# Kernel tuning notes

Measured on AMD Instinct MI355X. Metric: run time of the kernel, lower is better.

The kernel has to match this reference:

```python
import jax, jax.numpy as jnp
import numpy as np

N, D, H, T = 262144, 128, 256, 4  # nodes, embed_dim, hidden_dim, num node types


def setup_inputs() -> dict:
    key = jax.random.key(0)
    ks = jax.random.split(key, 5)
    h = jax.random.normal(ks[0], (N, D), dtype=jnp.float32)
    message = jax.random.normal(ks[1], (N, D), dtype=jnp.float32)
    node_type_ids = jax.random.randint(ks[2], (N,), 0, T, dtype=jnp.int32)
    # Spectrally-normalized linear weights are just fixed matrices at eval time;
    # scale so spectral norm is O(1).
    W1 = jax.random.normal(ks[3], (T, 2 * D, H), dtype=jnp.float32) / np.sqrt(2 * D)
    b1 = jnp.zeros((T, H), dtype=jnp.float32)
    W2 = jax.random.normal(ks[4], (T, H, D), dtype=jnp.float32) / np.sqrt(H)
    b2 = jnp.zeros((T, D), dtype=jnp.float32)
    return {"h": h, "message": message, "node_type_ids": node_type_ids,
            "W1": W1, "b1": b1, "W2": W2, "b2": b2}


def reference(h, message, node_type_ids, W1, b1, W2, b2):
    # x : (N, 2d) concatenated node state and message
    x = jnp.concatenate([h, message], axis=-1)
    dh = jnp.zeros_like(h)
    # Loop over the small fixed set of node types (T=4); each iteration is a
    # dense 2-layer SiLU MLP, results routed back by boolean mask (the torch
    # code's gather -> MLP -> scatter, expressed as compute-all + select).
    for t in range(T):
        y = jax.nn.silu(x @ W1[t] + b1[t]) @ W2[t] + b2[t]  # (N, d)
        mask = (node_type_ids == t)[:, None]
        dh = jnp.where(mask, y, dh)
    return dh
```

## Files before the change

### kernel.cpp

```cpp
#include <hip/hip_runtime.h>
#include <hip/hip_bf16.h>
#include <stdint.h>

#define N_NODES 262144
#define DDIM 128
#define KDIM 256
#define HDIM 256
#define NTYPE 4
#define BM 64
#define NB 1024

typedef float  f32x4  __attribute__((ext_vector_type(4)));
typedef short  bf16x8 __attribute__((ext_vector_type(8)));
typedef unsigned short u16x4 __attribute__((ext_vector_type(4)));


__device__ __forceinline__ unsigned short f2b(float v) {
    unsigned int u = __builtin_bit_cast(unsigned int, v);
    u += 0x7FFFu + ((u >> 16) & 1u);
    return (unsigned short)(u >> 16);
}

__global__ void k_prep_hist(const int* __restrict__ ids,
                            const float* __restrict__ W1, const float* __restrict__ W2,
                            int* __restrict__ bcnt,
                            unsigned short* __restrict__ W1T, unsigned short* __restrict__ W2T) {
    __shared__ int cnt[NTYPE];
    if (blockIdx.x < NB) {
        int tid = threadIdx.x, lane = tid & 63;
        if (tid < NTYPE) cnt[tid] = 0;
        __syncthreads();
        int t = ids[blockIdx.x * 256 + tid];
        #pragma unroll
        for (int tt = 0; tt < NTYPE; ++tt) {
            unsigned long long m = __ballot(t == tt);
            if (lane == 0) atomicAdd(&cnt[tt], (int)__popcll(m));
        }
        __syncthreads();
        if (tid < NTYPE) bcnt[tid * NB + blockIdx.x] = cnt[tid];
    } else {
        int tid = (blockIdx.x - NB) * 256 + threadIdx.x;
        const int stride = 256 * 256;
        const int n1 = NTYPE * HDIM * KDIM;
        for (int i = tid; i < n1; i += stride) {
            int t = i / (HDIM * KDIM);
            int rem = i % (HDIM * KDIM);
            int hh = rem / KDIM;
            int k  = rem % KDIM;
            W1T[i] = f2b(W1[((size_t)t * KDIM + k) * HDIM + hh]);
        }
        const int n2 = NTYPE * DDIM * HDIM;
        for (int i = tid; i < n2; i += stride) {
            int t = i / (DDIM * HDIM);
            int rem = i % (DDIM * HDIM);
            int d = rem / HDIM;
            int k = rem % HDIM;
            W2T[i] = f2b(W2[((size_t)t * HDIM + k) * DDIM + d]);
        }
    }
}

__global__ __launch_bounds__(1024) void k_scan(const int* __restrict__ bcnt,
                                               int* __restrict__ gbase, int* __restrict__ meta) {
    __shared__ int wpart[16];
    __shared__ int ttot[NTYPE + 1];
    int tid = threadIdx.x, lane = tid & 63, wv = tid >> 6;
    if (tid == 0) ttot[0] = 0;
    for (int t = 0; t < NTYPE; ++t) {
        int v = bcnt[t * NB + tid];
        int s = v;
        #pragma unroll
        for (int d = 1; d < 64; d <<= 1) {
            int u = __shfl_up(s, d, 64);
            if (lane >= d) s += u;
        }
        if (lane == 63) wpart[wv] = s;
        __syncthreads();
        if (tid == 0) {
            int a = 0;
            for (int w = 0; w < 16; ++w) { int x = wpart[w]; wpart[w] = a; a += x; }
            ttot[t + 1] = ttot[t] + a;
        }
        __syncthreads();
        gbase[t * NB + tid] = ttot[t] + wpart[wv] + (s - v);
        __syncthreads();
    }
    if (tid == 0) {
        int off = 0, toff = 0;
        for (int t = 0; t < NTYPE; ++t) {
            int c = ttot[t + 1] - ttot[t];
            meta[4 + t] = off;
            meta[9 + t] = toff;
            off  += c;
            toff += (c + BM - 1) / BM;
        }
        meta[8]  = off;
        meta[13] = toff;
    }
}

__global__ void k_scatter(const int* __restrict__ ids, const int* __restrict__ gbase,
                          int* __restrict__ perm) {
    __shared__ int wb[4][NTYPE];
    int tid = threadIdx.x, lane = tid & 63, wv = tid >> 6;
    int i = blockIdx.x * 256 + tid;
    int t = ids[i];
    #pragma unroll
    for (int tt = 0; tt < NTYPE; ++tt) {
        unsigned long long m = __ballot(t == tt);
        if (lane == 0) wb[wv][tt] = (int)__popcll(m);
    }
    __syncthreads();
    if (tid < NTYPE) {
        int a = 0;
        for (int w = 0; w < 4; ++w) { int x = wb[w][tid]; wb[w][tid] = a; a += x; }
    }
    __syncthreads();
    #pragma unroll
    for (int tt = 0; tt < NTYPE; ++tt) {
        unsigned long long m = __ballot(t == tt);
        if (t == tt) {
            int rank = (int)__popcll(m & ((1ull << lane) - 1ull));
            perm[gbase[tt * NB + blockIdx.x] + wb[wv][tt] + rank] = i;
        }
    }
}

__global__ __launch_bounds__(256, 2) void k_mlp(
        const float* __restrict__ hbuf, const float* __restrict__ mbuf,
        const float* __restrict__ b1,   const float* __restrict__ b2,
        const int* __restrict__ meta,   const int* __restrict__ perm,
        const unsigned short* __restrict__ W1T, const unsigned short* __restrict__ W2T,
        float* __restrict__ dh) {
    __shared__ unsigned short xls[BM * KDIM];
    __shared__ unsigned short als[BM * HDIM];

    int b = blockIdx.x;
    if (b >= meta[13]) return;
    int t = 0;
    #pragma unroll
    for (int tt = 1; tt < NTYPE; ++tt) t += (b >= meta[9 + tt]);
    int row0   = meta[4 + t] + (b - meta[9 + t]) * BM;
    int segend = meta[4 + t + 1];

    int tid = threadIdx.x, lane = tid & 63, w = tid >> 6;
    int lr = lane & 15, lg = lane >> 4;

    int c = lane;
    #pragma unroll
    for (int j = 0; j < 16; ++j) {
        int r = w + 4 * j;
        int p = row0 + r;
        int node = perm[p < N_NODES ? p : N_NODES - 1];
        const float* src = (c < 32) ? (hbuf + (size_t)node * DDIM + c * 4)
                                    : (mbuf + (size_t)node * DDIM + (c - 32) * 4);
        float4 v = *reinterpret_cast<const float4*>(src);
        u16x4 o;
        o.x = f2b(v.x); o.y = f2b(v.y); o.z = f2b(v.z); o.w = f2b(v.w);
        int soff = (r * KDIM + c * 4) ^ ((r & 7) << 3);
        *reinterpret_cast<u16x4*>(&xls[soff]) = o;
    }

    f32x4 acc[4][4];
    #pragma unroll
    for (int ht = 0; ht < 4; ++ht)
        #pragma unroll
        for (int mt = 0; mt < 4; ++mt)
            acc[ht][mt] = (f32x4){0.f, 0.f, 0.f, 0.f};

    const unsigned short* W1p = W1T + ((size_t)t * HDIM + w * 64) * KDIM;
    __syncthreads();

    #pragma unroll
    for (int kh = 0; kh < 2; ++kh) {
        bf16x8 aw[4][4];
        #pragma unroll
        for (int ht = 0; ht < 4; ++ht)
            #pragma unroll
            for (int kt = 0; kt < 4; ++kt)
                aw[ht][kt] = *reinterpret_cast<const bf16x8*>(
                    W1p + (size_t)(ht * 16 + lr) * KDIM + (kh * 4 + kt) * 32 + lg * 8);
        #pragma unroll
        for (int kt = 0; kt < 4; ++kt) {
            int kk = (kh * 4 + kt) * 32 + lg * 8;
            bf16x8 xb[4];
            #pragma unroll
            for (int mt = 0; mt < 4; ++mt) {
                int m = mt * 16 + lr;
                int soff = (m * KDIM + kk) ^ ((m & 7) << 3);
                xb[mt] = *reinterpret_cast<const bf16x8*>(&xls[soff]);
            }
            #pragma unroll
            for (int ht = 0; ht < 4; ++ht)
                #pragma unroll
                for (int mt = 0; mt < 4; ++mt)
                    acc[ht][mt] = __builtin_amdgcn_mfma_f32_16x16x32_bf16(aw[ht][kt], xb[mt], acc[ht][mt], 0, 0, 0);
        }
    }

    #pragma unroll
    for (int ht = 0; ht < 4; ++ht) {
        int h0 = w * 64 + ht * 16 + lg * 4;
        f32x4 b1v = *reinterpret_cast<const f32x4*>(&b1[t * HDIM + h0]);
        #pragma unroll
        for (int mt = 0; mt < 4; ++mt) {
            int m = mt * 16 + lr;
            u16x4 o;
            #pragma unroll
            for (int r4 = 0; r4 < 4; ++r4) {
                float z = acc[ht][mt][r4] + b1v[r4];
                float s = z / (1.f + __expf(-z));
                o[r4] = f2b(s);
            }
            int soff = (m * HDIM + h0) ^ ((m & 7) << 3);
            *reinterpret_cast<u16x4*>(&als[soff]) = o;
        }
    }

    const unsigned short* W2p = W2T + ((size_t)t * DDIM + w * 32) * HDIM;
    bf16x8 aw2[2][8];
    #pragma unroll
    for (int dt = 0; dt < 2; ++dt)
        #pragma unroll
        for (int kt = 0; kt < 8; ++kt)
            aw2[dt][kt] = *reinterpret_cast<const bf16x8*>(
                W2p + (size_t)(dt * 16 + lr) * HDIM + kt * 32 + lg * 8);
    int nd[4];
    #pragma unroll
    for (int mt = 0; mt < 4; ++mt) {
        int p = row0 + mt * 16 + lr;
        nd[mt] = perm[p < N_NODES ? p : N_NODES - 1];
    }
    __syncthreads();

    f32x4 acc2[2][4];
    #pragma unroll
    for (int dt = 0; dt < 2; ++dt)
        #pragma unroll
        for (int mt = 0; mt < 4; ++mt)
            acc2[dt][mt] = (f32x4){0.f, 0.f, 0.f, 0.f};
    #pragma unroll
    for (int kt = 0; kt < 8; ++kt) {
        int kk = kt * 32 + lg * 8;
        bf16x8 ab[4];
        #pragma unroll
        for (int mt = 0; mt < 4; ++mt) {
            int m = mt * 16 + lr;
            int soff = (m * HDIM + kk) ^ ((m & 7) << 3);
            ab[mt] = *reinterpret_cast<const bf16x8*>(&als[soff]);
        }
        #pragma unroll
        for (int dt = 0; dt < 2; ++dt)
            #pragma unroll
            for (int mt = 0; mt < 4; ++mt)
                acc2[dt][mt] = __builtin_amdgcn_mfma_f32_16x16x32_bf16(aw2[dt][kt], ab[mt], acc2[dt][mt], 0, 0, 0);
    }

    #pragma unroll
    for (int dt = 0; dt < 2; ++dt) {
        int d0 = w * 32 + dt * 16 + lg * 4;
        f32x4 b2v = *reinterpret_cast<const f32x4*>(&b2[t * DDIM + d0]);
        #pragma unroll
        for (int mt = 0; mt < 4; ++mt) {
            int p = row0 + mt * 16 + lr;
            if (p < segend) {
                f32x4 v = acc2[dt][mt] + b2v;
                *reinterpret_cast<f32x4*>(&dh[(size_t)nd[mt] * DDIM + d0]) = v;
            }
        }
    }
}

extern "C" void kernel_launch(void* const* d_in, const int* in_sizes, int n_in,
                              void* d_out, int out_size, void* d_ws, size_t ws_size,
                              hipStream_t stream) {
    const float* h   = (const float*)d_in[0];
    const float* msg = (const float*)d_in[1];
    const int*   ids = (const int*)d_in[2];
    const float* W1  = (const float*)d_in[3];
    const float* b1  = (const float*)d_in[4];
    const float* W2  = (const float*)d_in[5];
    const float* b2  = (const float*)d_in[6];
    float* dh = (float*)d_out;

    char* ws = (char*)d_ws;
    int* meta  = (int*)ws;
    int* perm  = (int*)(ws + 128);
    int* bcnt  = (int*)(ws + 128 + (size_t)N_NODES * 4);
    int* gbase = bcnt + NTYPE * NB;
    unsigned short* W1T = (unsigned short*)(gbase + NTYPE * NB);
    unsigned short* W2T = W1T + (size_t)NTYPE * HDIM * KDIM;

    k_prep_hist<<<NB + 256, 256, 0, stream>>>(ids, W1, W2, bcnt, W1T, W2T);
    k_scan<<<1, 1024, 0, stream>>>(bcnt, gbase, meta);
    k_scatter<<<NB, 256, 0, stream>>>(ids, gbase, perm);
    k_mlp<<<N_NODES / BM + NTYPE, 256, 0, stream>>>(h, msg, b1, b2, meta, perm, W1T, W2T, dh);
}
```

Baseline: 446.4 us.

## Share one LDS buffer and stream weights per k-step to raise occupancy

The input and activation tiles now share a single 32KB shared buffer instead of two, with extra barriers so the activation tile can overwrite the input tile. Weights are loaded per k-step instead of prefetched in large register arrays, and launch bounds are raised to four blocks per SIMD. Type and row metadata and the gathered node index are made wave-uniform with readfirstlane. The aim is higher occupancy to hide gather and weight-load latency, at the cost of less register-level prefetch and more barriers.

```diff
diff --git a/kernel.cpp b/kernel.cpp
--- a/kernel.cpp
+++ b/kernel.cpp
@@ -126,22 +126,22 @@
     }
 }
 
-__global__ __launch_bounds__(256, 2) void k_mlp(
+__global__ __launch_bounds__(256, 4) void k_mlp(
         const float* __restrict__ hbuf, const float* __restrict__ mbuf,
         const float* __restrict__ b1,   const float* __restrict__ b2,
         const int* __restrict__ meta,   const int* __restrict__ perm,
         const unsigned short* __restrict__ W1T, const unsigned short* __restrict__ W2T,
         float* __restrict__ dh) {
-    __shared__ unsigned short xls[BM * KDIM];
-    __shared__ unsigned short als[BM * HDIM];
+    __shared__ unsigned short lsb[BM * KDIM];
 
     int b = blockIdx.x;
     if (b >= meta[13]) return;
     int t = 0;
     #pragma unroll
     for (int tt = 1; tt < NTYPE; ++tt) t += (b >= meta[9 + tt]);
-    int row0   = meta[4 + t] + (b - meta[9 + t]) * BM;
-    int segend = meta[4 + t + 1];
+    t = __builtin_amdgcn_readfirstlane(t);
+    int row0   = __builtin_amdgcn_readfirstlane(meta[4 + t] + (b - meta[9 + t]) * BM);
+    int segend = __builtin_amdgcn_readfirstlane(meta[4 + t + 1]);
 
     int tid = threadIdx.x, lane = tid & 63, w = tid >> 6;
     int lr = lane & 15, lg = lane >> 4;
@@ -151,15 +151,16 @@
     for (int j = 0; j < 16; ++j) {
         int r = w + 4 * j;
         int p = row0 + r;
-        int node = perm[p < N_NODES ? p : N_NODES - 1];
+        int node = __builtin_amdgcn_readfirstlane(perm[p < N_NODES ? p : N_NODES - 1]);
         const float* src = (c < 32) ? (hbuf + (size_t)node * DDIM + c * 4)
                                     : (mbuf + (size_t)node * DDIM + (c - 32) * 4);
         float4 v = *reinterpret_cast<const float4*>(src);
         u16x4 o;
         o.x = f2b(v.x); o.y = f2b(v.y); o.z = f2b(v.z); o.w = f2b(v.w);
         int soff = (r * KDIM + c * 4) ^ ((r & 7) << 3);
-        *reinterpret_cast<u16x4*>(&xls[soff]) = o;
-    }
+        *reinterpret_cast<u16x4*>(&lsb[soff]) = o;
+    }
+    __syncthreads();
 
     f32x4 acc[4][4];
     #pragma unroll
@@ -169,34 +170,26 @@
             acc[ht][mt] = (f32x4){0.f, 0.f, 0.f, 0.f};
 
     const unsigned short* W1p = W1T + ((size_t)t * HDIM + w * 64) * KDIM;
-    __syncthreads();
-
-    #pragma unroll
-    for (int kh = 0; kh < 2; ++kh) {
-        bf16x8 aw[4][4];
+    #pragma unroll
+    for (int kt = 0; kt < KDIM / 32; ++kt) {
+        int kk = kt * 32 + lg * 8;
+        bf16x8 aw[4], xb[4];
+        #pragma unroll
+        for (int ht = 0; ht < 4; ++ht)
+            aw[ht] = *reinterpret_cast<const bf16x8*>(W1p + (size_t)(ht * 16 + lr) * KDIM + kk);
+        #pragma unroll
+        for (int mt = 0; mt < 4; ++mt) {
+            int m = mt * 16 + lr;
+            int soff = (m * KDIM + kk) ^ ((m & 7) << 3);
+            xb[mt] = *reinterpret_cast<const bf16x8*>(&lsb[soff]);
+        }
         #pragma unroll
         for (int ht = 0; ht < 4; ++ht)
             #pragma unroll
-            for (int kt = 0; kt < 4; ++kt)
-                aw[ht][kt] = *reinterpret_cast<const bf16x8*>(
-                    W1p + (size_t)(ht * 16 + lr) * KDIM + (kh * 4 + kt) * 32 + lg * 8);
-        #pragma unroll
-        for (int kt = 0; kt < 4; ++kt) {
-            int kk = (kh * 4 + kt) * 32 + lg * 8;
-            bf16x8 xb[4];
-            #pragma unroll
-            for (int mt = 0; mt < 4; ++mt) {
-                int m = mt * 16 + lr;
-                int soff = (m * KDIM + kk) ^ ((m & 7) << 3);
-                xb[mt] = *reinterpret_cast<const bf16x8*>(&xls[soff]);
-            }
-            #pragma unroll
-            for (int ht = 0; ht < 4; ++ht)
-                #pragma unroll
-                for (int mt = 0; mt < 4; ++mt)
-                    acc[ht][mt] = __builtin_amdgcn_mfma_f32_16x16x32_bf16(aw[ht][kt], xb[mt], acc[ht][mt], 0, 0, 0);
-        }
-    }
+            for (int mt = 0; mt < 4; ++mt)
+                acc[ht][mt] = __builtin_amdgcn_mfma_f32_16x16x32_bf16(aw[ht], xb[mt], acc[ht][mt], 0, 0, 0);
+    }
+    __syncthreads();
 
     #pragma unroll
     for (int ht = 0; ht < 4; ++ht) {
@@ -213,49 +206,45 @@
                 o[r4] = f2b(s);
             }
             int soff = (m * HDIM + h0) ^ ((m & 7) << 3);
-            *reinterpret_cast<u16x4*>(&als[soff]) = o;
-        }
-    }
+            *reinterpret_cast<u16x4*>(&lsb[soff]) = o;
+        }
+    }
+    __syncthreads();
+
+    f32x4 acc2[2][4];
+    #pragma unroll
+    for (int dt = 0; dt < 2; ++dt)
+        #pragma unroll
+        for (int mt = 0; mt < 4; ++mt)
+            acc2[dt][mt] = (f32x4){0.f, 0.f, 0.f, 0.f};
 
     const unsigned short* W2p = W2T + ((size_t)t * DDIM + w * 32) * HDIM;
-    bf16x8 aw2[2][8];
-    #pragma unroll
-    for (int dt = 0; dt < 2; ++dt)
-        #pragma unroll
-        for (int kt = 0; kt < 8; ++kt)
-            aw2[dt][kt] = *reinterpret_cast<const bf16x8*>(
-                W2p + (size_t)(dt * 16 + lr) * HDIM + kt * 32 + lg * 8);
+    #pragma unroll
+    for (int kt = 0; kt < HDIM / 32; ++kt) {
+        int kk = kt * 32 + lg * 8;
+        bf16x8 aw2[2], ab[4];
+        #pragma unroll
+        for (int dt = 0; dt < 2; ++dt)
+            aw2[dt] = *reinterpret_cast<const bf16x8*>(W2p + (size_t)(dt * 16 + lr) * HDIM + kk);
+        #pragma unroll
+        for (int mt = 0; mt < 4; ++mt) {
+            int m = mt * 16 + lr;
+            int soff = (m * HDIM + kk) ^ ((m & 7) << 3);
+            ab[mt] = *reinterpret_cast<const bf16x8*>(&lsb[soff]);
+        }
+        #pragma unroll
+        for (int dt = 0; dt < 2; ++dt)
+            #pragma unroll
+            for (int mt = 0; mt < 4; ++mt)
+                acc2[dt][mt] = __builtin_amdgcn_mfma_f32_16x16x32_bf16(aw2[dt], ab[mt], acc2[dt][mt], 0, 0, 0);
+    }
+
     int nd[4];
     #pragma unroll
     for (int mt = 0; mt < 4; ++mt) {
         int p = row0 + mt * 16 + lr;
         nd[mt] = perm[p < N_NODES ? p : N_NODES - 1];
     }
-    __syncthreads();
-
-    f32x4 acc2[2][4];
-    #pragma unroll
-    for (int dt = 0; dt < 2; ++dt)
-        #pragma unroll
-        for (int mt = 0; mt < 4; ++mt)
-            acc2[dt][mt] = (f32x4){0.f, 0.f, 0.f, 0.f};
-    #pragma unroll
-    for (int kt = 0; kt < 8; ++kt) {
-        int kk = kt * 32 + lg * 8;
-        bf16x8 ab[4];
-        #pragma unroll
-        for (int mt = 0; mt < 4; ++mt) {
-            int m = mt * 16 + lr;
-            int soff = (m * HDIM + kk) ^ ((m & 7) << 3);
-            ab[mt] = *reinterpret_cast<const bf16x8*>(&als[soff]);
-        }
-        #pragma unroll
-        for (int dt = 0; dt < 2; ++dt)
-            #pragma unroll
-            for (int mt = 0; mt < 4; ++mt)
-                acc2[dt][mt] = __builtin_amdgcn_mfma_f32_16x16x32_bf16(aw2[dt][kt], ab[mt], acc2[dt][mt], 0, 0, 0);
-    }
-
     #pragma unroll
     for (int dt = 0; dt < 2; ++dt) {
         int d0 = w * 32 + dt * 16 + lg * 4;
```

After: 446.1 us. No clear change (-0.0%).
